# Kernel optimization log

Hardware: AMD Instinct MI355X
Metric: run time of the kernel (lower is better)

## Reference

```python
import jax, jax.numpy as jnp
import numpy as np


def setup_inputs() -> dict:
    key = jax.random.key(0)
    k1, k2 = jax.random.split(key)
    B, S, D = 8, 4096, 1024
    E, P = 8, 4
    x = jax.random.normal(k1, (B, S, D), dtype=jnp.float32)
    phi_kernel = jax.random.normal(k2, (D, E * P), dtype=jnp.float32) * (1.0 / np.sqrt(D))
    phi_bias = jnp.zeros((E * P,), dtype=jnp.float32)
    return {"x": x, "phi_kernel": phi_kernel, "phi_bias": phi_bias,
            "num_experts": E, "num_slots": P}


def reference(x, phi_kernel, phi_bias, num_experts, num_slots):
    B, S, D = x.shape
    E, P = num_experts, num_slots
    # phi logits: [B,S,E,P]
    phi_logits = (jnp.einsum('bsd,dk->bsk', x, phi_kernel) + phi_bias).reshape(B, S, E, P)
    # softmax over the sequence axis (each slot is a convex combo of tokens)
    phi_weights = jax.nn.softmax(phi_logits, axis=1)
    # soft slots: weighted sum over tokens -> [B,E,P,D] (fused, no [B,S,E,P,D] blowup)
    soft_slots = jnp.einsum('bsd,bsep->bepd', x, phi_weights)
    expert_inputs = soft_slots.reshape(B, E, P * D)
    expert_weights = jnp.full((B, S, E), 1.0 / E, dtype=x.dtype)
    expert_indices = jnp.broadcast_to(jnp.arange(E, dtype=jnp.int32)[None, None, :], (B, S, E))
    return (expert_weights, expert_indices, phi_weights, soft_slots, expert_inputs)
```

## Files before the change

kernel.cpp:

```cpp
#include <hip/hip_runtime.h>
#include <hip/hip_bf16.h>

#define B 8
#define S 4096
#define DD 1024
#define KK 32

typedef __attribute__((ext_vector_type(8))) short bf16x8;
typedef __attribute__((ext_vector_type(16))) float f32x16;

static __device__ __forceinline__ unsigned short f2bf(float f) {
    unsigned int u = __builtin_bit_cast(unsigned int, f);
    u += 0x7FFFu + ((u >> 16) & 1u);
    return (unsigned short)(u >> 16);
}

__global__ __launch_bounds__(256) void k0_phit(const float* __restrict__ phi,
                                               unsigned short* __restrict__ phiT) {
    __shared__ float lt[32][33];
    const int d0 = blockIdx.x * 32;
    const int tid = threadIdx.x;
#pragma unroll
    for (int i = 0; i < 4; ++i) {
        int slot = tid + i * 256;
        int d = slot >> 5, k = slot & 31;
        lt[d][k] = phi[(size_t)(d0 + d) * KK + k];
    }
    __syncthreads();
    const int k = tid >> 3, c = tid & 7, d = c * 4;
    short4 pk;
    pk.x = (short)f2bf(lt[d + 0][k]);
    pk.y = (short)f2bf(lt[d + 1][k]);
    pk.z = (short)f2bf(lt[d + 2][k]);
    pk.w = (short)f2bf(lt[d + 3][k]);
    *(short4*)(phiT + (size_t)k * DD + d0 + d) = pk;
}

__global__ __launch_bounds__(256) void k1_logits(const float* __restrict__ x,
                                                 const unsigned short* __restrict__ phiT,
                                                 const float* __restrict__ bias,
                                                 float* __restrict__ lp) {
    __shared__ __align__(16) char sm[32768 + 2 * 16384];

    const int bid = blockIdx.x;
    const int dq = bid & 1;
    const int st = (bid >> 1) & 31;
    const int b  = bid >> 6;
    const int s0 = st * 128;
    const int tid = threadIdx.x;
    const int wv = __builtin_amdgcn_readfirstlane(tid >> 6);
    const int lane = tid & 63;
    const int l31 = lane & 31;
    const int half = lane >> 5;

    {
        const uint4* pg = (const uint4*)phiT;
#pragma unroll
        for (int i = 0; i < 8; ++i) {
            int slot = tid + i * 256;
            int k = slot >> 6, blk = slot & 63;
            uint4 v = pg[(size_t)k * 128 + dq * 64 + blk];
            *(uint4*)(sm + (size_t)k * 1024 + ((blk ^ (k & 7)) << 4)) = v;
        }
    }

    f32x16 acc;
    {
        float bv = (dq == 0) ? bias[l31] : 0.f;
#pragma unroll
        for (int r = 0; r < 16; ++r) acc[r] = bv;
    }

    const float* xg = x + ((size_t)(b * S + s0)) * DD + dq * 512;

    float4 q[8];
    auto load8 = [&](int ch) {
#pragma unroll
        for (int i = 0; i < 8; ++i) {
            int slot = tid + i * 256;
            int s = slot >> 4, c4 = slot & 15;
            q[i] = *(const float4*)(xg + (size_t)s * DD + ch * 64 + c4 * 4);
        }
    };
    auto store8 = [&](char* buf) {
#pragma unroll
        for (int i = 0; i < 8; ++i) {
            int slot = tid + i * 256;
            int s = slot >> 4, c4 = slot & 15;
            short4 pk;
            pk.x = (short)f2bf(q[i].x);
            pk.y = (short)f2bf(q[i].y);
            pk.z = (short)f2bf(q[i].z);
            pk.w = (short)f2bf(q[i].w);
            *(short4*)(buf + (size_t)s * 128 + (((c4 >> 1) ^ (s & 7)) << 4) + (c4 & 1) * 8) = pk;
        }
    };

    load8(0);
    store8(sm + 32768);
    __syncthreads();

    const int srow = wv * 32 + l31;
    const int sx = srow & 7;
    const int kx = l31 & 7;

    for (int ch = 0; ch < 8; ++ch) {
        char* cur = sm + 32768 + (ch & 1) * 16384;
        char* nxt = sm + 32768 + ((ch & 1) ^ 1) * 16384;
        if (ch < 7) load8(ch + 1);
#pragma unroll
        for (int step = 0; step < 4; ++step) {
            int blk = step * 2 + half;
            bf16x8 af  = *(const bf16x8*)(cur + (size_t)srow * 128 + ((blk ^ sx) << 4));
            bf16x8 bfv = *(const bf16x8*)(sm + (size_t)l31 * 1024 + (((ch * 8 + blk) ^ kx) << 4));
            acc = __builtin_amdgcn_mfma_f32_32x32x16_bf16(af, bfv, acc, 0, 0, 0);
        }
        __syncthreads();
        if (ch < 7) store8(nxt);
        __syncthreads();
    }

    float* lt = (float*)(sm + 32768);
#pragma unroll
    for (int r = 0; r < 16; ++r) {
        int row = (r & 3) + 8 * (r >> 2) + 4 * half;
        lt[(size_t)l31 * 129 + wv * 32 + row] = acc[r];
    }
    __syncthreads();
    float* o = lp + ((size_t)(dq * B + b) * KK) * S + s0;
#pragma unroll
    for (int i = 0; i < 4; ++i) {
        int slot = tid + i * 256;
        int k = slot >> 5, s4 = slot & 31;
        float4 v;
        v.x = lt[k * 129 + s4 * 4 + 0];
        v.y = lt[k * 129 + s4 * 4 + 1];
        v.z = lt[k * 129 + s4 * 4 + 2];
        v.w = lt[k * 129 + s4 * 4 + 3];
        *(float4*)(o + (size_t)k * S + s4 * 4) = v;
    }
}

__global__ __launch_bounds__(256) void k2a_partial(const float* __restrict__ lp,
                                                   float* __restrict__ pmax,
                                                   float* __restrict__ psum) {
    const int bid = blockIdx.x;
    const int c  = bid & 7;
    const int bk = bid >> 3;
    const int tid = threadIdx.x;
    const int wave = tid >> 6, lane = tid & 63;
    const size_t base = (size_t)bk * S + c * 512;

    float v0 = lp[base + tid]       + lp[1048576 + base + tid];
    float v1 = lp[base + tid + 256] + lp[1048576 + base + tid + 256];

    float m = fmaxf(v0, v1);
#pragma unroll
    for (int off = 32; off >= 1; off >>= 1) m = fmaxf(m, __shfl_xor(m, off, 64));
    __shared__ float sm_[4], sl[4];
    if (lane == 0) sm_[wave] = m;
    __syncthreads();
    const float M = fmaxf(fmaxf(sm_[0], sm_[1]), fmaxf(sm_[2], sm_[3]));

    float l = __expf(v0 - M) + __expf(v1 - M);
#pragma unroll
    for (int off = 32; off >= 1; off >>= 1) l += __shfl_xor(l, off, 64);
    if (lane == 0) sl[wave] = l;
    __syncthreads();
    if (tid == 0) {
        pmax[bid] = M;
        psum[bid] = sl[0] + sl[1] + sl[2] + sl[3];
    }
}

__global__ __launch_bounds__(256) void k2c_norm(const float* __restrict__ lp,
                                                const float* __restrict__ pmax,
                                                const float* __restrict__ psum,
                                                unsigned short* __restrict__ wbT,
                                                float* __restrict__ pw_out) {
    __shared__ float tile[128][33];
    __shared__ float sM[32], sLinv[32];
    const int b  = blockIdx.x >> 5;
    const int sc = blockIdx.x & 31;
    const int s0 = sc * 128;
    const int tid = threadIdx.x;

    if (tid < 32) {
        const int k = tid;
        float M = -1e30f, L = 0.f;
#pragma unroll
        for (int c = 0; c < 8; ++c) {
            float mc = pmax[(b * KK + k) * 8 + c];
            float lc = psum[(b * KK + k) * 8 + c];
            float nM = fmaxf(M, mc);
            L = L * __expf(M - nM) + lc * __expf(mc - nM);
            M = nM;
        }
        sM[k] = M;
        sLinv[k] = 1.0f / L;
    }
    __syncthreads();

    const int sL = tid & 127;
    const int kh = tid >> 7;
#pragma unroll
    for (int kk = 0; kk < 16; ++kk) {
        const int k = kk * 2 + kh;
        const size_t idx = ((size_t)b * KK + k) * S + s0 + sL;
        float v = lp[idx] + lp[1048576 + idx];
        float w = __expf(v - sM[k]) * sLinv[k];
        wbT[idx] = f2bf(w);
        tile[sL][k] = w;
    }
    __syncthreads();

    float* ob = pw_out + ((size_t)b * S + s0) * KK;
#pragma unroll
    for (int i = 0; i < 4; ++i) {
        const int idx4 = tid + i * 256;
        const int sl = idx4 >> 3, kq = idx4 & 7;
        float4 v4 = make_float4(tile[sl][kq * 4 + 0], tile[sl][kq * 4 + 1],
                                tile[sl][kq * 4 + 2], tile[sl][kq * 4 + 3]);
        ((float4*)ob)[idx4] = v4;
    }
}

__global__ __launch_bounds__(256) void k3_slots(const float* __restrict__ x,
                                                const unsigned int* __restrict__ wbT32,
                                                float* __restrict__ part) {
    __shared__ __align__(16) char sm[2 * 16384 + 2 * 4096];

    const int bid = blockIdx.x;
    const int sc = bid & 7;
    const int dg = (bid >> 3) & 7;
    const int b  = bid >> 6;
    const int tid = threadIdx.x;
    const int wv = __builtin_amdgcn_readfirstlane(tid >> 6);
    const int lane = tid & 63;
    const int l31 = lane & 31;
    const int half = lane >> 5;

    const int dth = tid & 127;
    const int sh  = tid >> 7;

    const float* xg = x + ((size_t)(b * S + sc * 512)) * DD + dg * 128 + dth;
    const unsigned int* wg = wbT32 + (size_t)b * KK * (S / 2) + sc * 256;

    float q0[16], q1[16];
    unsigned int qw[4];
    auto loadc = [&](int ch) {
#pragma unroll
        for (int j = 0; j < 16; ++j) {
            int sp = sh * 16 + j;
            q0[j] = xg[(size_t)(ch * 64 + sp * 2) * DD];
            q1[j] = xg[(size_t)(ch * 64 + sp * 2 + 1) * DD];
        }
#pragma unroll
        for (int i = 0; i < 4; ++i) {
            int slot = tid + i * 256;
            int k = slot >> 5, c = slot & 31;
            qw[i] = wg[(size_t)k * (S / 2) + ch * 32 + c];
        }
    };
    auto storec = [&](char* xB, char* wB) {
#pragma unroll
        for (int j = 0; j < 16; ++j) {
            int sp = sh * 16 + j;
            unsigned int pkd = (unsigned int)f2bf(q0[j]) | ((unsigned int)f2bf(q1[j]) << 16);
            *(unsigned int*)(xB + (size_t)dth * 128 + (((sp >> 2) ^ (dth & 7)) << 4) + (sp & 3) * 4) = pkd;
        }
#pragma unroll
        for (int i = 0; i < 4; ++i) {
            int slot = tid + i * 256;
            int k = slot >> 5, c = slot & 31;
            *(unsigned int*)(wB + (size_t)k * 128 + (((c >> 2) ^ (k & 7)) << 4) + (c & 3) * 4) = qw[i];
        }
    };

    f32x16 acc;
#pragma unroll
    for (int r = 0; r < 16; ++r) acc[r] = 0.f;

    loadc(0);
    storec(sm, sm + 32768);
    __syncthreads();

    const int dloc = wv * 32 + l31;
    const int dx = dloc & 7;
    const int kx = l31 & 7;

    for (int ch = 0; ch < 8; ++ch) {
        const int cur = ch & 1;
        char* xCur = sm + cur * 16384;
        char* wCur = sm + 32768 + cur * 4096;
        char* xNxt = sm + (cur ^ 1) * 16384;
        char* wNxt = sm + 32768 + (cur ^ 1) * 4096;
        if (ch < 7) loadc(ch + 1);
#pragma unroll
        for (int step = 0; step < 4; ++step) {
            int blk = step * 2 + half;
            bf16x8 af  = *(const bf16x8*)(wCur + (size_t)l31 * 128 + ((blk ^ kx) << 4));
            bf16x8 bfv = *(const bf16x8*)(xCur + (size_t)dloc * 128 + ((blk ^ dx) << 4));
            acc = __builtin_amdgcn_mfma_f32_32x32x16_bf16(af, bfv, acc, 0, 0, 0);
        }
        __syncthreads();
        if (ch < 7) storec(xNxt, wNxt);
        __syncthreads();
    }

    float* pp = part + (((size_t)sc * B + b) * KK) * DD + dg * 128 + wv * 32 + l31;
#pragma unroll
    for (int r = 0; r < 16; ++r) {
        int k = (r & 3) + 8 * (r >> 2) + 4 * half;
        pp[(size_t)k * DD] = acc[r];
    }
}

__global__ __launch_bounds__(256) void k4_finalize(const float* __restrict__ part,
                                                   float* __restrict__ out) {
    const int idx = blockIdx.x * 256 + threadIdx.x;
    const float4* p4 = (const float4*)part;

    float4 sv = p4[idx];
#pragma unroll
    for (int c = 1; c < 8; ++c) {
        float4 t = p4[(size_t)c * 65536 + idx];
        sv.x += t.x; sv.y += t.y; sv.z += t.z; sv.w += t.w;
    }

    ((float4*)(out + 1572864))[idx] = sv;
    ((float4*)(out + 1835008))[idx] = sv;
    ((float4*)out)[idx] = make_float4(0.125f, 0.125f, 0.125f, 0.125f);
    float base = (float)((idx * 4) & 7);
    ((float4*)(out + 262144))[idx] = make_float4(base, base + 1.f, base + 2.f, base + 3.f);
}

extern "C" void kernel_launch(void* const* d_in, const int* in_sizes, int n_in,
                              void* d_out, int out_size, void* d_ws, size_t ws_size,
                              hipStream_t stream) {
    const float* x    = (const float*)d_in[0];
    const float* phi  = (const float*)d_in[1];
    const float* bias = (const float*)d_in[2];
    float* out = (float*)d_out;

    float* ws = (float*)d_ws;
    float* lp   = ws;
    float* pmax = ws + 2097152;
    float* psum = ws + 2099200;
    unsigned short* wbT  = (unsigned short*)(ws + 2101248);
    unsigned short* phiT = (unsigned short*)(ws + 2625536);
    float* part = ws + 2641920;
    float* pw_out = out + 524288;

    k0_phit<<<dim3(32), dim3(256), 0, stream>>>(phi, phiT);
    k1_logits<<<dim3(512), dim3(256), 0, stream>>>(x, phiT, bias, lp);
    k2a_partial<<<dim3(2048), dim3(256), 0, stream>>>(lp, pmax, psum);
    k2c_norm<<<dim3(256), dim3(256), 0, stream>>>(lp, pmax, psum, wbT, pw_out);
    k3_slots<<<dim3(512), dim3(256), 0, stream>>>(x, (const unsigned int*)wbT, part);
    k4_finalize<<<dim3(256), dim3(256), 0, stream>>>(part, out);
}
```

Before: 234.0 us.

## Fuse partial softmax stats into logits kernel and drop D-split

The logits kernel no longer splits D into two halves. Each block now covers the full D over 16 chunks, writes a single logits buffer, and computes the per-128-token max and sum-exp itself. That removes the k2a_partial launch and the extra pass that added the two partial logit buffers. The phi and weight B-operands are now read straight from global memory instead of being staged in LDS. This frees shared memory but turns those operand fetches into uncoalesced global loads. The logits kernel also launches half as many blocks, so each does twice the serial work, which lowers parallelism across the GPU.

Measured after the change: 276.2 us. +18.0%, slower.

```diff
diff --git a/kernel.cpp b/kernel.cpp
--- a/kernel.cpp
+++ b/kernel.cpp
@@ -39,13 +39,14 @@
 __global__ __launch_bounds__(256) void k1_logits(const float* __restrict__ x,
                                                  const unsigned short* __restrict__ phiT,
                                                  const float* __restrict__ bias,
-                                                 float* __restrict__ lp) {
-    __shared__ __align__(16) char sm[32768 + 2 * 16384];
+                                                 float* __restrict__ lp,
+                                                 float* __restrict__ pmax,
+                                                 float* __restrict__ psum) {
+    __shared__ __align__(16) char sm[32768];
 
     const int bid = blockIdx.x;
-    const int dq = bid & 1;
-    const int st = (bid >> 1) & 31;
-    const int b  = bid >> 6;
+    const int st = bid & 31;
+    const int b  = bid >> 5;
     const int s0 = st * 128;
     const int tid = threadIdx.x;
     const int wv = __builtin_amdgcn_readfirstlane(tid >> 6);
@@ -53,25 +54,14 @@
     const int l31 = lane & 31;
     const int half = lane >> 5;
 
-    {
-        const uint4* pg = (const uint4*)phiT;
-#pragma unroll
-        for (int i = 0; i < 8; ++i) {
-            int slot = tid + i * 256;
-            int k = slot >> 6, blk = slot & 63;
-            uint4 v = pg[(size_t)k * 128 + dq * 64 + blk];
-            *(uint4*)(sm + (size_t)k * 1024 + ((blk ^ (k & 7)) << 4)) = v;
-        }
-    }
-
     f32x16 acc;
     {
-        float bv = (dq == 0) ? bias[l31] : 0.f;
+        float bv = bias[l31];
 #pragma unroll
         for (int r = 0; r < 16; ++r) acc[r] = bv;
     }
 
-    const float* xg = x + ((size_t)(b * S + s0)) * DD + dq * 512;
+    const float* xg = x + ((size_t)(b * S + s0)) * DD;
 
     float4 q[8];
     auto load8 = [&](int ch) {
@@ -97,37 +87,70 @@
     };
 
     load8(0);
-    store8(sm + 32768);
+    store8(sm);
     __syncthreads();
 
     const int srow = wv * 32 + l31;
     const int sx = srow & 7;
-    const int kx = l31 & 7;
-
-    for (int ch = 0; ch < 8; ++ch) {
-        char* cur = sm + 32768 + (ch & 1) * 16384;
-        char* nxt = sm + 32768 + ((ch & 1) ^ 1) * 16384;
-        if (ch < 7) load8(ch + 1);
+    const char* pgb = (const char*)phiT + (size_t)l31 * 2048;
+
+    for (int ch = 0; ch < 16; ++ch) {
+        char* cur = sm + (ch & 1) * 16384;
+        char* nxt = sm + ((ch & 1) ^ 1) * 16384;
+        if (ch < 15) load8(ch + 1);
 #pragma unroll
         for (int step = 0; step < 4; ++step) {
             int blk = step * 2 + half;
             bf16x8 af  = *(const bf16x8*)(cur + (size_t)srow * 128 + ((blk ^ sx) << 4));
-            bf16x8 bfv = *(const bf16x8*)(sm + (size_t)l31 * 1024 + (((ch * 8 + blk) ^ kx) << 4));
+            bf16x8 bfv = *(const bf16x8*)(pgb + ch * 128 + (blk << 4));
             acc = __builtin_amdgcn_mfma_f32_32x32x16_bf16(af, bfv, acc, 0, 0, 0);
         }
         __syncthreads();
-        if (ch < 7) store8(nxt);
-        __syncthreads();
-    }
-
-    float* lt = (float*)(sm + 32768);
+        if (ch < 15) store8(nxt);
+        __syncthreads();
+    }
+
+    float* lt   = (float*)sm;
+    float* red  = (float*)(sm + 16512);
+    float* sMk  = (float*)(sm + 16512 + 1024);
 #pragma unroll
     for (int r = 0; r < 16; ++r) {
         int row = (r & 3) + 8 * (r >> 2) + 4 * half;
         lt[(size_t)l31 * 129 + wv * 32 + row] = acc[r];
     }
     __syncthreads();
-    float* o = lp + ((size_t)(dq * B + b) * KK) * S + s0;
+
+    {
+        const int k = tid >> 3, seg = tid & 7;
+        const float* row = lt + (size_t)k * 129 + seg * 16;
+        float m = row[0];
+#pragma unroll
+        for (int i = 1; i < 16; ++i) m = fmaxf(m, row[i]);
+        red[tid] = m;
+        __syncthreads();
+        if (tid < 32) {
+            float M = red[tid * 8];
+#pragma unroll
+            for (int j = 1; j < 8; ++j) M = fmaxf(M, red[tid * 8 + j]);
+            sMk[tid] = M;
+        }
+        __syncthreads();
+        float M = sMk[k];
+        float l = 0.f;
+#pragma unroll
+        for (int i = 0; i < 16; ++i) l += __expf(row[i] - M);
+        red[tid] = l;
+        __syncthreads();
+        if (tid < 32) {
+            float L = 0.f;
+#pragma unroll
+            for (int j = 0; j < 8; ++j) L += red[tid * 8 + j];
+            pmax[((size_t)b * KK + tid) * 32 + st] = sMk[tid];
+            psum[((size_t)b * KK + tid) * 32 + st] = L;
+        }
+    }
+
+    float* o = lp + ((size_t)b * KK) * S + s0;
 #pragma unroll
     for (int i = 0; i < 4; ++i) {
         int slot = tid + i * 256;
@@ -138,38 +161,6 @@
         v.z = lt[k * 129 + s4 * 4 + 2];
         v.w = lt[k * 129 + s4 * 4 + 3];
         *(float4*)(o + (size_t)k * S + s4 * 4) = v;
-    }
-}
-
-__global__ __launch_bounds__(256) void k2a_partial(const float* __restrict__ lp,
-                                                   float* __restrict__ pmax,
-                                                   float* __restrict__ psum) {
-    const int bid = blockIdx.x;
-    const int c  = bid & 7;
-    const int bk = bid >> 3;
-    const int tid = threadIdx.x;
-    const int wave = tid >> 6, lane = tid & 63;
-    const size_t base = (size_t)bk * S + c * 512;
-
-    float v0 = lp[base + tid]       + lp[1048576 + base + tid];
-    float v1 = lp[base + tid + 256] + lp[1048576 + base + tid + 256];
-
-    float m = fmaxf(v0, v1);
-#pragma unroll
-    for (int off = 32; off >= 1; off >>= 1) m = fmaxf(m, __shfl_xor(m, off, 64));
-    __shared__ float sm_[4], sl[4];
-    if (lane == 0) sm_[wave] = m;
-    __syncthreads();
-    const float M = fmaxf(fmaxf(sm_[0], sm_[1]), fmaxf(sm_[2], sm_[3]));
-
-    float l = __expf(v0 - M) + __expf(v1 - M);
-#pragma unroll
-    for (int off = 32; off >= 1; off >>= 1) l += __shfl_xor(l, off, 64);
-    if (lane == 0) sl[wave] = l;
-    __syncthreads();
-    if (tid == 0) {
-        pmax[bid] = M;
-        psum[bid] = sl[0] + sl[1] + sl[2] + sl[3];
     }
 }
 
@@ -189,9 +180,9 @@
         const int k = tid;
         float M = -1e30f, L = 0.f;
 #pragma unroll
-        for (int c = 0; c < 8; ++c) {
-            float mc = pmax[(b * KK + k) * 8 + c];
-            float lc = psum[(b * KK + k) * 8 + c];
+        for (int c = 0; c < 32; ++c) {
+            float mc = pmax[((size_t)b * KK + k) * 32 + c];
+            float lc = psum[((size_t)b * KK + k) * 32 + c];
             float nM = fmaxf(M, mc);
             L = L * __expf(M - nM) + lc * __expf(mc - nM);
             M = nM;
@@ -207,8 +198,7 @@
     for (int kk = 0; kk < 16; ++kk) {
         const int k = kk * 2 + kh;
         const size_t idx = ((size_t)b * KK + k) * S + s0 + sL;
-        float v = lp[idx] + lp[1048576 + idx];
-        float w = __expf(v - sM[k]) * sLinv[k];
+        float w = __expf(lp[idx] - sM[k]) * sLinv[k];
         wbT[idx] = f2bf(w);
         tile[sL][k] = w;
     }
@@ -226,9 +216,9 @@
 }
 
 __global__ __launch_bounds__(256) void k3_slots(const float* __restrict__ x,
-                                                const unsigned int* __restrict__ wbT32,
+                                                const unsigned short* __restrict__ wbT,
                                                 float* __restrict__ part) {
-    __shared__ __align__(16) char sm[2 * 16384 + 2 * 4096];
+    __shared__ __align__(16) char sm[32768];
 
     const int bid = blockIdx.x;
     const int sc = bid & 7;
@@ -244,10 +234,8 @@
     const int sh  = tid >> 7;
 
     const float* xg = x + ((size_t)(b * S + sc * 512)) * DD + dg * 128 + dth;
-    const unsigned int* wg = wbT32 + (size_t)b * KK * (S / 2) + sc * 256;
 
     float q0[16], q1[16];
-    unsigned int qw[4];
     auto loadc = [&](int ch) {
 #pragma unroll
         for (int j = 0; j < 16; ++j) {
@@ -255,26 +243,14 @@
             q0[j] = xg[(size_t)(ch * 64 + sp * 2) * DD];
             q1[j] = xg[(size_t)(ch * 64 + sp * 2 + 1) * DD];
         }
-#pragma unroll
-        for (int i = 0; i < 4; ++i) {
-            int slot = tid + i * 256;
-            int k = slot >> 5, c = slot & 31;
-            qw[i] = wg[(size_t)k * (S / 2) + ch * 32 + c];
-        }
     };
-    auto storec = [&](char* xB, char* wB) {
+    auto storec = [&](char* xB) {
 #pragma unroll
         for (int j = 0; j < 16; ++j) {
             int sp = sh * 16 + j;
             unsigned int pkd = (unsigned int)f2bf(q0[j]) | ((unsigned int)f2bf(q1[j]) << 16);
             *(unsigned int*)(xB + (size_t)dth * 128 + (((sp >> 2) ^ (dth & 7)) << 4) + (sp & 3) * 4) = pkd;
         }
-#pragma unroll
-        for (int i = 0; i < 4; ++i) {
-            int slot = tid + i * 256;
-            int k = slot >> 5, c = slot & 31;
-            *(unsigned int*)(wB + (size_t)k * 128 + (((c >> 2) ^ (k & 7)) << 4) + (c & 3) * 4) = qw[i];
-        }
     };
 
     f32x16 acc;
@@ -282,29 +258,26 @@
     for (int r = 0; r < 16; ++r) acc[r] = 0.f;
 
     loadc(0);
-    storec(sm, sm + 32768);
+    storec(sm);
     __syncthreads();
 
     const int dloc = wv * 32 + l31;
     const int dx = dloc & 7;
-    const int kx = l31 & 7;
+    const char* wgb = (const char*)wbT + ((size_t)(b * KK + l31) * S + sc * 512) * 2;
 
     for (int ch = 0; ch < 8; ++ch) {
-        const int cur = ch & 1;
-        char* xCur = sm + cur * 16384;
-        char* wCur = sm + 32768 + cur * 4096;
-        char* xNxt = sm + (cur ^ 1) * 16384;
-        char* wNxt = sm + 32768 + (cur ^ 1) * 4096;
+        char* cur = sm + (ch & 1) * 16384;
+        char* nxt = sm + ((ch & 1) ^ 1) * 16384;
         if (ch < 7) loadc(ch + 1);
 #pragma unroll
         for (int step = 0; step < 4; ++step) {
             int blk = step * 2 + half;
-            bf16x8 af  = *(const bf16x8*)(wCur + (size_t)l31 * 128 + ((blk ^ kx) << 4));
-            bf16x8 bfv = *(const bf16x8*)(xCur + (size_t)dloc * 128 + ((blk ^ dx) << 4));
+            bf16x8 af  = *(const bf16x8*)(wgb + ch * 128 + (blk << 4));
+            bf16x8 bfv = *(const bf16x8*)(cur + (size_t)dloc * 128 + ((blk ^ dx) << 4));
             acc = __builtin_amdgcn_mfma_f32_32x32x16_bf16(af, bfv, acc, 0, 0, 0);
         }
         __syncthreads();
-        if (ch < 7) storec(xNxt, wNxt);
+        if (ch < 7) storec(nxt);
         __syncthreads();
     }
 
@@ -345,17 +318,16 @@
 
     float* ws = (float*)d_ws;
     float* lp   = ws;
-    float* pmax = ws + 2097152;
-    float* psum = ws + 2099200;
-    unsigned short* wbT  = (unsigned short*)(ws + 2101248);
-    unsigned short* phiT = (unsigned short*)(ws + 2625536);
-    float* part = ws + 2641920;
+    float* pmax = ws + 1048576;
+    float* psum = ws + 1056768;
+    unsigned short* wbT  = (unsigned short*)(ws + 1064960);
+    unsigned short* phiT = (unsigned short*)(ws + 1589248);
+    float* part = ws + 1605632;
     float* pw_out = out + 524288;
 
     k0_phit<<<dim3(32), dim3(256), 0, stream>>>(phi, phiT);
-    k1_logits<<<dim3(512), dim3(256), 0, stream>>>(x, phiT, bias, lp);
-    k2a_partial<<<dim3(2048), dim3(256), 0, stream>>>(lp, pmax, psum);
+    k1_logits<<<dim3(256), dim3(256), 0, stream>>>(x, phiT, bias, lp, pmax, psum);
     k2c_norm<<<dim3(256), dim3(256), 0, stream>>>(lp, pmax, psum, wbT, pw_out);
-    k3_slots<<<dim3(512), dim3(256), 0, stream>>>(x, (const unsigned int*)wbT, part);
+    k3_slots<<<dim3(512), dim3(256), 0, stream>>>(x, wbT, part);
     k4_finalize<<<dim3(256), dim3(256), 0, stream>>>(part, out);
 }
```

## Split D across four logits blocks and S across sixteen slot blocks, load B operands to registers

Applied to the files above, without the earlier changes.

The logits kernel now splits the D reduction four ways instead of two, doubling its grid and shrinking shared memory. It loads the phi operand straight from global into registers instead of staging it in LDS. The slot kernel likewise halves its sequence chunk to double its grid and loads the softmax weights straight into registers. The aim is more blocks and occupancy across the many CUs, less LDS and fewer syncs. In exchange there are more partial buffers to write and reduce in the softmax and finalize kernels, which adds memory traffic.

After: 240.0 us. +2.6%, slower.

```diff
diff --git a/kernel.cpp b/kernel.cpp
--- a/kernel.cpp
+++ b/kernel.cpp
@@ -40,12 +40,12 @@
                                                  const unsigned short* __restrict__ phiT,
                                                  const float* __restrict__ bias,
                                                  float* __restrict__ lp) {
-    __shared__ __align__(16) char sm[32768 + 2 * 16384];
+    __shared__ __align__(16) char sm[32768];
 
     const int bid = blockIdx.x;
-    const int dq = bid & 1;
-    const int st = (bid >> 1) & 31;
-    const int b  = bid >> 6;
+    const int dq = bid & 3;
+    const int st = (bid >> 2) & 31;
+    const int b  = bid >> 7;
     const int s0 = st * 128;
     const int tid = threadIdx.x;
     const int wv = __builtin_amdgcn_readfirstlane(tid >> 6);
@@ -53,17 +53,6 @@
     const int l31 = lane & 31;
     const int half = lane >> 5;
 
-    {
-        const uint4* pg = (const uint4*)phiT;
-#pragma unroll
-        for (int i = 0; i < 8; ++i) {
-            int slot = tid + i * 256;
-            int k = slot >> 6, blk = slot & 63;
-            uint4 v = pg[(size_t)k * 128 + dq * 64 + blk];
-            *(uint4*)(sm + (size_t)k * 1024 + ((blk ^ (k & 7)) << 4)) = v;
-        }
-    }
-
     f32x16 acc;
     {
         float bv = (dq == 0) ? bias[l31] : 0.f;
@@ -71,7 +60,8 @@
         for (int r = 0; r < 16; ++r) acc[r] = bv;
     }
 
-    const float* xg = x + ((size_t)(b * S + s0)) * DD + dq * 512;
+    const float* xg = x + ((size_t)(b * S + s0)) * DD + dq * 256;
+    const char* pgb = (const char*)phiT + (size_t)l31 * 2048 + dq * 512;
 
     float4 q[8];
     auto load8 = [&](int ch) {
@@ -96,38 +86,54 @@
         }
     };
 
+    bf16x8 pf[4];
+    auto loadphi = [&](bf16x8* dst, int ch) {
+#pragma unroll
+        for (int t = 0; t < 4; ++t)
+            dst[t] = *(const bf16x8*)(pgb + ch * 128 + (((t * 2 + half)) << 4));
+    };
+
     load8(0);
-    store8(sm + 32768);
+    loadphi(pf, 0);
+    store8(sm);
     __syncthreads();
 
     const int srow = wv * 32 + l31;
     const int sx = srow & 7;
-    const int kx = l31 & 7;
-
-    for (int ch = 0; ch < 8; ++ch) {
-        char* cur = sm + 32768 + (ch & 1) * 16384;
-        char* nxt = sm + 32768 + ((ch & 1) ^ 1) * 16384;
-        if (ch < 7) load8(ch + 1);
+
+#pragma unroll
+    for (int ch = 0; ch < 4; ++ch) {
+        char* cur = sm + (ch & 1) * 16384;
+        char* nxt = sm + ((ch & 1) ^ 1) * 16384;
+        bf16x8 npf[4];
+        if (ch < 3) {
+            load8(ch + 1);
+            loadphi(npf, ch + 1);
+        }
 #pragma unroll
         for (int step = 0; step < 4; ++step) {
             int blk = step * 2 + half;
-            bf16x8 af  = *(const bf16x8*)(cur + (size_t)srow * 128 + ((blk ^ sx) << 4));
-            bf16x8 bfv = *(const bf16x8*)(sm + (size_t)l31 * 1024 + (((ch * 8 + blk) ^ kx) << 4));
-            acc = __builtin_amdgcn_mfma_f32_32x32x16_bf16(af, bfv, acc, 0, 0, 0);
+            bf16x8 af = *(const bf16x8*)(cur + (size_t)srow * 128 + ((blk ^ sx) << 4));
+            acc = __builtin_amdgcn_mfma_f32_32x32x16_bf16(af, pf[step], acc, 0, 0, 0);
         }
         __syncthreads();
-        if (ch < 7) store8(nxt);
+        if (ch < 3) {
+            store8(nxt);
+#pragma unroll
+            for (int t = 0; t < 4; ++t) pf[t] = npf[t];
+        }
         __syncthreads();
     }
 
-    float* lt = (float*)(sm + 32768);
+    float* lt = (float*)sm;
 #pragma unroll
     for (int r = 0; r < 16; ++r) {
         int row = (r & 3) + 8 * (r >> 2) + 4 * half;
         lt[(size_t)l31 * 129 + wv * 32 + row] = acc[r];
     }
     __syncthreads();
-    float* o = lp + ((size_t)(dq * B + b) * KK) * S + s0;
+
+    float* o = lp + (size_t)dq * (B * KK * S) + ((size_t)b * KK) * S + s0;
 #pragma unroll
     for (int i = 0; i < 4; ++i) {
         int slot = tid + i * 256;
@@ -151,8 +157,12 @@
     const int wave = tid >> 6, lane = tid & 63;
     const size_t base = (size_t)bk * S + c * 512;
 
-    float v0 = lp[base + tid]       + lp[1048576 + base + tid];
-    float v1 = lp[base + tid + 256] + lp[1048576 + base + tid + 256];
+    float v0 = 0.f, v1 = 0.f;
+#pragma unroll
+    for (int p = 0; p < 4; ++p) {
+        v0 += lp[(size_t)p * 1048576 + base + tid];
+        v1 += lp[(size_t)p * 1048576 + base + tid + 256];
+    }
 
     float m = fmaxf(v0, v1);
 #pragma unroll
@@ -178,11 +188,11 @@
                                                 const float* __restrict__ psum,
                                                 unsigned short* __restrict__ wbT,
                                                 float* __restrict__ pw_out) {
-    __shared__ float tile[128][33];
+    __shared__ float tile[64][33];
     __shared__ float sM[32], sLinv[32];
-    const int b  = blockIdx.x >> 5;
-    const int sc = blockIdx.x & 31;
-    const int s0 = sc * 128;
+    const int b  = blockIdx.x >> 6;
+    const int sc = blockIdx.x & 63;
+    const int s0 = sc * 64;
     const int tid = threadIdx.x;
 
     if (tid < 32) {
@@ -201,13 +211,15 @@
     }
     __syncthreads();
 
-    const int sL = tid & 127;
-    const int kh = tid >> 7;
-#pragma unroll
-    for (int kk = 0; kk < 16; ++kk) {
-        const int k = kk * 2 + kh;
+    const int sL = tid & 63;
+    const int kh = tid >> 6;
+#pragma unroll
+    for (int kk = 0; kk < 8; ++kk) {
+        const int k = kk * 4 + kh;
         const size_t idx = ((size_t)b * KK + k) * S + s0 + sL;
-        float v = lp[idx] + lp[1048576 + idx];
+        float v = 0.f;
+#pragma unroll
+        for (int p = 0; p < 4; ++p) v += lp[(size_t)p * 1048576 + idx];
         float w = __expf(v - sM[k]) * sLinv[k];
         wbT[idx] = f2bf(w);
         tile[sL][k] = w;
@@ -216,7 +228,7 @@
 
     float* ob = pw_out + ((size_t)b * S + s0) * KK;
 #pragma unroll
-    for (int i = 0; i < 4; ++i) {
+    for (int i = 0; i < 2; ++i) {
         const int idx4 = tid + i * 256;
         const int sl = idx4 >> 3, kq = idx4 & 7;
         float4 v4 = make_float4(tile[sl][kq * 4 + 0], tile[sl][kq * 4 + 1],
@@ -226,14 +238,14 @@
 }
 
 __global__ __launch_bounds__(256) void k3_slots(const float* __restrict__ x,
-                                                const unsigned int* __restrict__ wbT32,
+                                                const unsigned short* __restrict__ wbT,
                                                 float* __restrict__ part) {
-    __shared__ __align__(16) char sm[2 * 16384 + 2 * 4096];
+    __shared__ __align__(16) char sm[32768];
 
     const int bid = blockIdx.x;
-    const int sc = bid & 7;
-    const int dg = (bid >> 3) & 7;
-    const int b  = bid >> 6;
+    const int sc = bid & 15;
+    const int dg = (bid >> 4) & 7;
+    const int b  = bid >> 7;
     const int tid = threadIdx.x;
     const int wv = __builtin_amdgcn_readfirstlane(tid >> 6);
     const int lane = tid & 63;
@@ -243,11 +255,10 @@
     const int dth = tid & 127;
     const int sh  = tid >> 7;
 
-    const float* xg = x + ((size_t)(b * S + sc * 512)) * DD + dg * 128 + dth;
-    const unsigned int* wg = wbT32 + (size_t)b * KK * (S / 2) + sc * 256;
+    const float* xg = x + ((size_t)(b * S + sc * 256)) * DD + dg * 128 + dth;
+    const char* wgb = (const char*)wbT + ((size_t)(b * KK + l31) * S + sc * 256) * 2;
 
     float q0[16], q1[16];
-    unsigned int qw[4];
     auto loadc = [&](int ch) {
 #pragma unroll
         for (int j = 0; j < 16; ++j) {
@@ -255,26 +266,20 @@
             q0[j] = xg[(size_t)(ch * 64 + sp * 2) * DD];
             q1[j] = xg[(size_t)(ch * 64 + sp * 2 + 1) * DD];
         }
-#pragma unroll
-        for (int i = 0; i < 4; ++i) {
-            int slot = tid + i * 256;
-            int k = slot >> 5, c = slot & 31;
-            qw[i] = wg[(size_t)k * (S / 2) + ch * 32 + c];
-        }
-    };
-    auto storec = [&](char* xB, char* wB) {
+    };
+    auto storec = [&](char* xB) {
 #pragma unroll
         for (int j = 0; j < 16; ++j) {
             int sp = sh * 16 + j;
             unsigned int pkd = (unsigned int)f2bf(q0[j]) | ((unsigned int)f2bf(q1[j]) << 16);
             *(unsigned int*)(xB + (size_t)dth * 128 + (((sp >> 2) ^ (dth & 7)) << 4) + (sp & 3) * 4) = pkd;
         }
-#pragma unroll
-        for (int i = 0; i < 4; ++i) {
-            int slot = tid + i * 256;
-            int k = slot >> 5, c = slot & 31;
-            *(unsigned int*)(wB + (size_t)k * 128 + (((c >> 2) ^ (k & 7)) << 4) + (c & 3) * 4) = qw[i];
-        }
+    };
+    bf16x8 wf[4];
+    auto loadw = [&](bf16x8* dst, int ch) {
+#pragma unroll
+        for (int t = 0; t < 4; ++t)
+            dst[t] = *(const bf16x8*)(wgb + ch * 128 + ((t * 2 + half) << 4));
     };
 
     f32x16 acc;
@@ -282,29 +287,34 @@
     for (int r = 0; r < 16; ++r) acc[r] = 0.f;
 
     loadc(0);
-    storec(sm, sm + 32768);
+    loadw(wf, 0);
+    storec(sm);
     __syncthreads();
 
     const int dloc = wv * 32 + l31;
     const int dx = dloc & 7;
-    const int kx = l31 & 7;
-
-    for (int ch = 0; ch < 8; ++ch) {
-        const int cur = ch & 1;
-        char* xCur = sm + cur * 16384;
-        char* wCur = sm + 32768 + cur * 4096;
-        char* xNxt = sm + (cur ^ 1) * 16384;
-        char* wNxt = sm + 32768 + (cur ^ 1) * 4096;
-        if (ch < 7) loadc(ch + 1);
+
+#pragma unroll
+    for (int ch = 0; ch < 4; ++ch) {
+        char* cur = sm + (ch & 1) * 16384;
+        char* nxt = sm + ((ch & 1) ^ 1) * 16384;
+        bf16x8 nwf[4];
+        if (ch < 3) {
+            loadc(ch + 1);
+            loadw(nwf, ch + 1);
+        }
 #pragma unroll
         for (int step = 0; step < 4; ++step) {
             int blk = step * 2 + half;
-            bf16x8 af  = *(const bf16x8*)(wCur + (size_t)l31 * 128 + ((blk ^ kx) << 4));
-            bf16x8 bfv = *(const bf16x8*)(xCur + (size_t)dloc * 128 + ((blk ^ dx) << 4));
-            acc = __builtin_amdgcn_mfma_f32_32x32x16_bf16(af, bfv, acc, 0, 0, 0);
+            bf16x8 bfv = *(const bf16x8*)(cur + (size_t)dloc * 128 + ((blk ^ dx) << 4));
+            acc = __builtin_amdgcn_mfma_f32_32x32x16_bf16(wf[step], bfv, acc, 0, 0, 0);
         }
         __syncthreads();
-        if (ch < 7) storec(xNxt, wNxt);
+        if (ch < 3) {
+            storec(nxt);
+#pragma unroll
+            for (int t = 0; t < 4; ++t) wf[t] = nwf[t];
+        }
         __syncthreads();
     }
 
@@ -319,20 +329,20 @@
 __global__ __launch_bounds__(256) void k4_finalize(const float* __restrict__ part,
                                                    float* __restrict__ out) {
     const int idx = blockIdx.x * 256 + threadIdx.x;
-    const float4* p4 = (const float4*)part;
-
-    float4 sv = p4[idx];
-#pragma unroll
-    for (int c = 1; c < 8; ++c) {
-        float4 t = p4[(size_t)c * 65536 + idx];
-        sv.x += t.x; sv.y += t.y; sv.z += t.z; sv.w += t.w;
-    }
-
-    ((float4*)(out + 1572864))[idx] = sv;
-    ((float4*)(out + 1835008))[idx] = sv;
-    ((float4*)out)[idx] = make_float4(0.125f, 0.125f, 0.125f, 0.125f);
-    float base = (float)((idx * 4) & 7);
-    ((float4*)(out + 262144))[idx] = make_float4(base, base + 1.f, base + 2.f, base + 3.f);
+    const float2* p2 = (const float2*)part;
+
+    float2 sv = p2[idx];
+#pragma unroll
+    for (int c = 1; c < 16; ++c) {
+        float2 t = p2[(size_t)c * 131072 + idx];
+        sv.x += t.x; sv.y += t.y;
+    }
+
+    ((float2*)(out + 1572864))[idx] = sv;
+    ((float2*)(out + 1835008))[idx] = sv;
+    ((float2*)out)[idx] = make_float2(0.125f, 0.125f);
+    float e0 = (float)((idx * 2) & 7);
+    ((float2*)(out + 262144))[idx] = make_float2(e0, e0 + 1.f);
 }
 
 extern "C" void kernel_launch(void* const* d_in, const int* in_sizes, int n_in,
@@ -345,17 +355,17 @@
 
     float* ws = (float*)d_ws;
     float* lp   = ws;
-    float* pmax = ws + 2097152;
-    float* psum = ws + 2099200;
-    unsigned short* wbT  = (unsigned short*)(ws + 2101248);
-    unsigned short* phiT = (unsigned short*)(ws + 2625536);
-    float* part = ws + 2641920;
+    float* pmax = ws + 4194304;
+    float* psum = ws + 4196352;
+    unsigned short* wbT  = (unsigned short*)(ws + 4198400);
+    unsigned short* phiT = (unsigned short*)(ws + 4722688);
+    float* part = ws + 4739072;
     float* pw_out = out + 524288;
 
     k0_phit<<<dim3(32), dim3(256), 0, stream>>>(phi, phiT);
-    k1_logits<<<dim3(512), dim3(256), 0, stream>>>(x, phiT, bias, lp);
+    k1_logits<<<dim3(1024), dim3(256), 0, stream>>>(x, phiT, bias, lp);
     k2a_partial<<<dim3(2048), dim3(256), 0, stream>>>(lp, pmax, psum);
-    k2c_norm<<<dim3(256), dim3(256), 0, stream>>>(lp, pmax, psum, wbT, pw_out);
-    k3_slots<<<dim3(512), dim3(256), 0, stream>>>(x, (const unsigned int*)wbT, part);
-    k4_finalize<<<dim3(256), dim3(256), 0, stream>>>(part, out);
-}
+    k2c_norm<<<dim3(512), dim3(256), 0, stream>>>(lp, pmax, psum, wbT, pw_out);
+    k3_slots<<<dim3(1024), dim3(256), 0, stream>>>(x, wbT, part);
+    k4_finalize<<<dim3(512), dim3(256), 0, stream>>>(part, out);
+}
```
